# Kernel tuning notes

Hardware: AMD Instinct MI355X
Metric: run time of the kernel (lower is better)

Reference implementation:

```python
import jax, jax.numpy as jnp
import numpy as np

NUM_HEADS = 12
SPARSITY = 0.5

def setup_inputs() -> dict:
    key = jax.random.key(0)
    ks = jax.random.split(key, 5)
    B, N, C = 16, 577, 768
    x = jax.random.normal(ks[0], (B, N, C), dtype=jnp.float32)
    x_original = jax.random.normal(ks[1], (B, N, C), dtype=jnp.float32)
    qkv_w = jax.random.normal(ks[2], (3 * C, C), dtype=jnp.float32) * (C ** -0.5)
    proj_w = jax.random.normal(ks[3], (C, C), dtype=jnp.float32) * (C ** -0.5)
    proj_b = jax.random.normal(ks[4], (C,), dtype=jnp.float32) * 0.01
    return {"x": x, "x_original": x_original, "qkv_w": qkv_w,
            "proj_w": proj_w, "proj_b": proj_b, "num_prop": 57}

def reference(x, x_original, qkv_w, proj_w, proj_b, num_prop):
    B, N, C = x.shape
    H = NUM_HEADS
    hd = C // H
    scale = hd ** -0.5
    # qkv projection (no bias): [B,N,3C] -> q,k,v each [B,H,N,hd]
    qkv = (x @ qkv_w.T).reshape(B, N, 3, H, hd).transpose(2, 0, 3, 1, 4)
    q, k, v = qkv[0], qkv[1], qkv[2]
    attn = jax.nn.softmax(jnp.einsum('bhnd,bhmd->bhnm', q * scale, k), axis=-1)
    # sparsity threshold: keep entries >= the int(N*N*sparsity)-th largest per (b,h)
    if SPARSITY < 1:
        flat = attn.reshape(B, H, N * N)
        desc = -jnp.sort(-flat, axis=-1)  # descending
        sigma = desc[:, :, int(N * N * SPARSITY)][:, :, None, None]
        attn = jnp.where(attn >= sigma, attn, jnp.zeros((), attn.dtype))
    if num_prop > 0:
        K = N - num_prop  # tokens kept (incl. CLS)
        # token importance: max over heads of attention diagonal (excluding CLS)
        diag = jnp.diagonal(attn, axis1=-2, axis2=-1)[:, :, 1:]  # [B,H,N-1]
        token_rank = jnp.argsort(-diag.max(axis=1), axis=1)      # [B,N-1] desc
        index_kept = token_rank[:, :N - 1 - num_prop] + 1        # [B,K-1]
        index_kept = jnp.concatenate(
            [jnp.zeros((B, 1), index_kept.dtype), index_kept], axis=1)  # [B,K]
        # gather kept query rows of attn: [B,H,K,N]
        idx = jnp.broadcast_to(index_kept[:, None, :, None], (B, H, K, N))
        attn_kept = jnp.take_along_axis(attn, idx, axis=2)
        x_original = jnp.take_along_axis(
            x_original, jnp.broadcast_to(index_kept[:, :, None], (B, K, C)), axis=1)
        out = jnp.einsum('bhkn,bhnd->bhkd', attn_kept, v)
        out = out.transpose(0, 2, 1, 3).reshape(B, K, C)
    else:
        out = jnp.einsum('bhnm,bhmd->bhnd', attn, v)
        out = out.transpose(0, 2, 1, 3).reshape(B, N, C)
    out = out @ proj_w.T + proj_b
    return (out, x_original)
```

## Files before the change

kernel.cpp:

```cpp
#include <hip/hip_runtime.h>
#include <cstdint>
#include <cstddef>


namespace {
constexpr int B_  = 16;
constexpr int N_  = 577;
constexpr int C_  = 768;
constexpr int H_  = 12;
constexpr int HD_ = 64;
constexpr int BH_ = B_ * H_;
constexpr int KK_ = N_ - 57;
constexpr unsigned KIDX_ = 166464u;
constexpr int M1_ = B_ * N_;
constexpr int M2_ = B_ * KK_;
}

__device__ __forceinline__ void fma4(const float4& a, const float4& b, float& acc) {
  acc = __builtin_fmaf(a.x, b.x, acc);
  acc = __builtin_fmaf(a.y, b.y, acc);
  acc = __builtin_fmaf(a.z, b.z, acc);
  acc = __builtin_fmaf(a.w, b.w, acc);
}

__global__ __launch_bounds__(256) void qkv_gemm(
    const float* __restrict__ X, const float* __restrict__ W,
    float* __restrict__ qb, float* __restrict__ kb, float* __restrict__ vb) {
  __shared__ __align__(16) float Xs[64][68];
  __shared__ __align__(16) float Ws2[128][68];
  const int m0 = blockIdx.x * 64;
  const int n0 = blockIdx.y * 128;
  const int t = threadIdx.x;
  const int tx = t & 15, ty = t >> 4;
  float acc[4][8] = {};
  for (int k0 = 0; k0 < 768; k0 += 64) {
    __syncthreads();
    {
      const int c = t & 15, r0 = t >> 4;
#pragma unroll
      for (int s = 0; s < 4; s++) {
        int r = r0 + 16 * s;
        int gm = m0 + r;
        float4 v = make_float4(0.f, 0.f, 0.f, 0.f);
        if (gm < M1_) v = *(const float4*)&X[(size_t)gm * 768 + k0 + 4 * c];
        *(float4*)&Xs[r][4 * c] = v;
      }
#pragma unroll
      for (int s = 0; s < 8; s++) {
        int r = r0 + 16 * s;
        float4 v = *(const float4*)&W[(size_t)(n0 + r) * 768 + k0 + 4 * c];
        *(float4*)&Ws2[r][4 * c] = v;
      }
    }
    __syncthreads();
#pragma unroll 2
    for (int d4 = 0; d4 < 16; d4++) {
      float4 a4[4], b4[8];
#pragma unroll
      for (int i = 0; i < 4; i++) a4[i] = *(const float4*)&Xs[tx + 16 * i][4 * d4];
#pragma unroll
      for (int j = 0; j < 8; j++) b4[j] = *(const float4*)&Ws2[ty + 16 * j][4 * d4];
#pragma unroll
      for (int i = 0; i < 4; i++)
#pragma unroll
        for (int j = 0; j < 8; j++) fma4(a4[i], b4[j], acc[i][j]);
    }
  }
  for (int i = 0; i < 4; i++) {
    int gm = m0 + tx + 16 * i;
    if (gm >= M1_) continue;
    int b = gm / N_, n = gm % N_;
    for (int j = 0; j < 8; j++) {
      int gn = n0 + ty + 16 * j;
      int which = gn / C_, rem = gn % C_;
      int h = rem >> 6, d = rem & 63;
      float* dst = (which == 0) ? qb : (which == 1) ? kb : vb;
      dst[(((size_t)(b * H_ + h)) * N_ + n) * HD_ + d] = acc[i][j];
    }
  }
}

__global__ __launch_bounds__(256) void attn_stats(
    const float* __restrict__ qb, const float* __restrict__ kb,
    float* __restrict__ rowmax_g, float* __restrict__ rowsum_g,
    float* __restrict__ ldiag) {
  __shared__ __align__(16) float Qs[64][68];
  __shared__ __align__(16) float Ksf[128][68];
  const int bh = blockIdx.x;
  const int q0 = blockIdx.y * 64;
  const int t = threadIdx.x;
  const int tx = t & 15, ty = t >> 4;
  {
    const int c = t & 15, r0 = t >> 4;
#pragma unroll
    for (int s = 0; s < 4; s++) {
      int r = r0 + 16 * s;
      int gq = q0 + r;
      float4 v = make_float4(0.f, 0.f, 0.f, 0.f);
      if (gq < N_) v = *(const float4*)&qb[((size_t)bh * N_ + gq) * HD_ + 4 * c];
      v.x *= 0.125f; v.y *= 0.125f; v.z *= 0.125f; v.w *= 0.125f;
      *(float4*)&Qs[r][4 * c] = v;
    }
  }
  float m[4], ss[4];
#pragma unroll
  for (int i = 0; i < 4; i++) { m[i] = -INFINITY; ss[i] = 0.f; }
  for (int n0 = 0; n0 < N_; n0 += 128) {
    __syncthreads();
    {
      const int c = t & 15, r0 = t >> 4;
#pragma unroll
      for (int s = 0; s < 8; s++) {
        int r = r0 + 16 * s;
        int gn = n0 + r;
        float4 v = make_float4(0.f, 0.f, 0.f, 0.f);
        if (gn < N_) v = *(const float4*)&kb[((size_t)bh * N_ + gn) * HD_ + 4 * c];
        *(float4*)&Ksf[r][4 * c] = v;
      }
    }
    __syncthreads();
    float l[4][8];
#pragma unroll
    for (int i = 0; i < 4; i++)
#pragma unroll
      for (int j = 0; j < 8; j++) l[i][j] = 0.f;
#pragma unroll 2
    for (int d4 = 0; d4 < 16; d4++) {
      float4 a4[4], b4[8];
#pragma unroll
      for (int i = 0; i < 4; i++) a4[i] = *(const float4*)&Qs[tx + 16 * i][4 * d4];
#pragma unroll
      for (int j = 0; j < 8; j++) b4[j] = *(const float4*)&Ksf[ty + 16 * j][4 * d4];
#pragma unroll
      for (int i = 0; i < 4; i++)
#pragma unroll
        for (int j = 0; j < 8; j++) fma4(a4[i], b4[j], l[i][j]);
    }
#pragma unroll
    for (int i = 0; i < 4; i++) {
      int gq = q0 + tx + 16 * i;
      float tmax = -INFINITY;
#pragma unroll
      for (int j = 0; j < 8; j++)
        if (n0 + ty + 16 * j < N_) tmax = fmaxf(tmax, l[i][j]);
      float mn = fmaxf(m[i], tmax);
      ss[i] *= expf(m[i] - mn);
#pragma unroll
      for (int j = 0; j < 8; j++) {
        int col = n0 + ty + 16 * j;
        if (col < N_) {
          ss[i] += expf(l[i][j] - mn);
          if (col == gq) ldiag[(size_t)bh * N_ + gq] = l[i][j];
        }
      }
      m[i] = mn;
    }
  }
  __syncthreads();
  float* Mred = &Ksf[0][0];
  float* Sred = &Ksf[0][0] + 1024;
#pragma unroll
  for (int i = 0; i < 4; i++) {
    int row = tx + 16 * i;
    Mred[row * 16 + ty] = m[i];
    Sred[row * 16 + ty] = ss[i];
  }
  __syncthreads();
  if (t < 64) {
    int gq = q0 + t;
    if (gq < N_) {
      float M = -INFINITY;
      for (int k = 0; k < 16; k++) M = fmaxf(M, Mred[t * 16 + k]);
      float S = 0.f;
      for (int k = 0; k < 16; k++) S += expf(Mred[t * 16 + k] - M) * Sred[t * 16 + k];
      rowmax_g[(size_t)bh * N_ + gq] = M;
      rowsum_g[(size_t)bh * N_ + gq] = S;
    }
  }
}

template <int MODE>
__global__ __launch_bounds__(256) void hist_pass(
    const float* __restrict__ qb, const float* __restrict__ kb,
    const float* __restrict__ rowmax_g, const float* __restrict__ rowsum_g,
    const unsigned* __restrict__ pfx_in, unsigned* __restrict__ hist_out) {
  constexpr int HB = (MODE == 2) ? 256 : 4096;
  __shared__ __align__(16) float Qs[64][68];
  __shared__ __align__(16) float Ksf[128][68];
  __shared__ unsigned hloc[HB];
  const int bh = blockIdx.x;
  const int q0 = blockIdx.y * 64;
  const int t = threadIdx.x;
  const int tx = t & 15, ty = t >> 4;
  for (int i = t; i < HB; i += 256) hloc[i] = 0u;
  const unsigned pf = (MODE == 0) ? 0u : pfx_in[bh];
  {
    const int c = t & 15, r0 = t >> 4;
#pragma unroll
    for (int s = 0; s < 4; s++) {
      int r = r0 + 16 * s;
      int gq = q0 + r;
      float4 v = make_float4(0.f, 0.f, 0.f, 0.f);
      if (gq < N_) v = *(const float4*)&qb[((size_t)bh * N_ + gq) * HD_ + 4 * c];
      v.x *= 0.125f; v.y *= 0.125f; v.z *= 0.125f; v.w *= 0.125f;
      *(float4*)&Qs[r][4 * c] = v;
    }
  }
  float M[4], inv[4];
#pragma unroll
  for (int i = 0; i < 4; i++) {
    int gq = q0 + tx + 16 * i;
    if (gq < N_) {
      M[i] = rowmax_g[(size_t)bh * N_ + gq];
      inv[i] = 1.f / rowsum_g[(size_t)bh * N_ + gq];
    } else { M[i] = 0.f; inv[i] = 0.f; }
  }
  for (int n0 = 0; n0 < N_; n0 += 128) {
    __syncthreads();
    {
      const int c = t & 15, r0 = t >> 4;
#pragma unroll
      for (int s = 0; s < 8; s++) {
        int r = r0 + 16 * s;
        int gn = n0 + r;
        float4 v = make_float4(0.f, 0.f, 0.f, 0.f);
        if (gn < N_) v = *(const float4*)&kb[((size_t)bh * N_ + gn) * HD_ + 4 * c];
        *(float4*)&Ksf[r][4 * c] = v;
      }
    }
    __syncthreads();
    float l[4][8];
#pragma unroll
    for (int i = 0; i < 4; i++)
#pragma unroll
      for (int j = 0; j < 8; j++) l[i][j] = 0.f;
#pragma unroll 2
    for (int d4 = 0; d4 < 16; d4++) {
      float4 a4[4], b4[8];
#pragma unroll
      for (int i = 0; i < 4; i++) a4[i] = *(const float4*)&Qs[tx + 16 * i][4 * d4];
#pragma unroll
      for (int j = 0; j < 8; j++) b4[j] = *(const float4*)&Ksf[ty + 16 * j][4 * d4];
#pragma unroll
      for (int i = 0; i < 4; i++)
#pragma unroll
        for (int j = 0; j < 8; j++) fma4(a4[i], b4[j], l[i][j]);
    }
#pragma unroll
    for (int i = 0; i < 4; i++) {
      int gq = q0 + tx + 16 * i;
#pragma unroll
      for (int j = 0; j < 8; j++) {
        bool valid = (gq < N_) && (n0 + ty + 16 * j < N_);
        if (MODE == 0) {
          unsigned bin = 0xFFFFu;
          if (valid) {
            float e = expf(l[i][j] - M[i]);
            float v = e * inv[i];
            bin = __float_as_uint(v) >> 20;
          }
          unsigned lead = (unsigned)__builtin_amdgcn_readfirstlane((int)bin);
          unsigned long long mm = __ballot(bin == lead);
          if (bin == lead) {
            if (lead != 0xFFFFu && (t & 63) == (__ffsll((unsigned long long)mm) - 1))
              atomicAdd(&hloc[lead], (unsigned)__popcll(mm));
          } else if (bin != 0xFFFFu) {
            atomicAdd(&hloc[bin], 1u);
          }
        } else if (valid) {
          float e = expf(l[i][j] - M[i]);
          float v = e * inv[i];
          unsigned bits = __float_as_uint(v);
          if (MODE == 1) {
            if ((bits >> 20) == pf) atomicAdd(&hloc[(bits >> 8) & 0xFFFu], 1u);
          } else {
            if ((bits >> 8) == pf) atomicAdd(&hloc[bits & 0xFFu], 1u);
          }
        }
      }
    }
  }
  __syncthreads();
  for (int i = t; i < HB; i += 256)
    if (hloc[i]) atomicAdd(&hist_out[(size_t)bh * HB + i], hloc[i]);
}

__global__ __launch_bounds__(64) void select_level(
    const unsigned* __restrict__ hist, int nbins,
    const unsigned* __restrict__ krem_in, const unsigned* __restrict__ pfx_in,
    unsigned* __restrict__ krem_out, unsigned* __restrict__ pfx_out, int shift) {
  const int bh = blockIdx.x;
  const int l = threadIdx.x;
  const int seg = nbins / 64;
  const unsigned krem = krem_in ? krem_in[bh] : KIDX_;
  const unsigned* hb = hist + (size_t)bh * nbins;
  __shared__ unsigned ps[64];
  unsigned psum = 0;
  int hi = nbins - 1 - l * seg;
  for (int i = 0; i < seg; i++) psum += hb[hi - i];
  ps[l] = psum;
  __syncthreads();
  if (l == 0) {
    unsigned cum = 0, before = 0;
    int bin = 0;
    for (int j = 0; j < 64; j++) {
      if (cum + ps[j] > krem) {
        unsigned c = cum;
        int hj = nbins - 1 - j * seg;
        for (int i = 0; i < seg; i++) {
          unsigned cnt = hb[hj - i];
          if (c + cnt > krem) { bin = hj - i; before = c; break; }
          c += cnt;
        }
        break;
      }
      cum += ps[j];
    }
    unsigned p = pfx_in ? pfx_in[bh] : 0u;
    pfx_out[bh] = (p << shift) | (unsigned)bin;
    krem_out[bh] = krem - before;
  }
}

__global__ __launch_bounds__(576) void rank_kernel(
    const float* __restrict__ ldiag, const float* __restrict__ rowmax_g,
    const float* __restrict__ rowsum_g, const unsigned* __restrict__ sigbits,
    int* __restrict__ kept) {
  const int b = blockIdx.x;
  const int i = threadIdx.x;
  __shared__ float sc[576];
  float s = 0.f;
  for (int h = 0; h < H_; h++) {
    int bh = b * H_ + h;
    float l = ldiag[(size_t)bh * N_ + (i + 1)];
    float M = rowmax_g[(size_t)bh * N_ + (i + 1)];
    float inv = 1.f / rowsum_g[(size_t)bh * N_ + (i + 1)];
    float e = expf(l - M);
    float v = e * inv;
    float sg = __uint_as_float(sigbits[bh]);
    if (v >= sg) s = fmaxf(s, v);
  }
  sc[i] = s;
  __syncthreads();
  int r = 0;
  for (int j = 0; j < 576; j++) {
    float sj = sc[j];
    if (sj > s || (sj == s && j < i)) r++;
  }
  if (r < KK_ - 1) kept[b * KK_ + r + 1] = i + 1;
  if (i == 0) kept[b * KK_] = 0;
}

__global__ __launch_bounds__(256) void gather_x(
    const float* __restrict__ xo, const int* __restrict__ kept,
    float* __restrict__ out2) {
  const int bp = blockIdx.x;
  const int b = bp / KK_, p = bp % KK_;
  const int src = kept[b * KK_ + p];
  const float* s = xo + ((size_t)b * N_ + src) * C_;
  float* d = out2 + (size_t)bp * C_;
  for (int c = threadIdx.x; c < C_; c += 256) d[c] = s[c];
}

__global__ __launch_bounds__(256) void av_kernel(
    const float* __restrict__ qb, const float* __restrict__ kb,
    const float* __restrict__ vb, const int* __restrict__ kept,
    const float* __restrict__ rowmax_g, const float* __restrict__ rowsum_g,
    const unsigned* __restrict__ sigbits, float* __restrict__ out1) {
  __shared__ __align__(16) float Qs[64][68];
  __shared__ __align__(16) float Ksf[64][68];
  __shared__ __align__(16) float Vs[64][68];
  __shared__ int ridx[64];
  __shared__ float Ml[64], Il[64];
  const int bh = blockIdx.x;
  const int p0 = blockIdx.y * 64;
  const int b = bh / H_, h = bh % H_;
  const float sigma = __uint_as_float(sigbits[bh]);
  const int t = threadIdx.x;
  const int tx = t & 15, ty = t >> 4;
  if (t < 64) {
    int pp = p0 + t;
    int r = (pp < KK_) ? kept[b * KK_ + pp] : 0;
    ridx[t] = r;
    Ml[t] = rowmax_g[(size_t)bh * N_ + r];
    Il[t] = 1.f / rowsum_g[(size_t)bh * N_ + r];
  }
  __syncthreads();
  {
    const int c = t & 15, r0 = t >> 4;
#pragma unroll
    for (int s = 0; s < 4; s++) {
      int r = r0 + 16 * s;
      int gq = ridx[r];
      float4 v = *(const float4*)&qb[((size_t)bh * N_ + gq) * HD_ + 4 * c];
      v.x *= 0.125f; v.y *= 0.125f; v.z *= 0.125f; v.w *= 0.125f;
      *(float4*)&Qs[r][4 * c] = v;
    }
  }
  float M[4], inv[4];
#pragma unroll
  for (int i = 0; i < 4; i++) { int row = tx + 16 * i; M[i] = Ml[row]; inv[i] = Il[row]; }
  float acc[4][4] = {};
  for (int n0 = 0; n0 < N_; n0 += 64) {
    __syncthreads();
    {
      const int c = t & 15, r0 = t >> 4;
#pragma unroll
      for (int s = 0; s < 4; s++) {
        int r = r0 + 16 * s;
        int gn = n0 + r;
        float4 kv = make_float4(0.f, 0.f, 0.f, 0.f);
        float4 vv = make_float4(0.f, 0.f, 0.f, 0.f);
        if (gn < N_) {
          kv = *(const float4*)&kb[((size_t)bh * N_ + gn) * HD_ + 4 * c];
          vv = *(const float4*)&vb[((size_t)bh * N_ + gn) * HD_ + 4 * c];
        }
        *(float4*)&Ksf[r][4 * c] = kv;
        *(float4*)&Vs[r][4 * c] = vv;
      }
    }
    __syncthreads();
    float l[4][4];
#pragma unroll
    for (int i = 0; i < 4; i++)
#pragma unroll
      for (int j = 0; j < 4; j++) l[i][j] = 0.f;
#pragma unroll 4
    for (int d4 = 0; d4 < 16; d4++) {
      float4 a4[4], b4[4];
#pragma unroll
      for (int i = 0; i < 4; i++) a4[i] = *(const float4*)&Qs[tx + 16 * i][4 * d4];
#pragma unroll
      for (int j = 0; j < 4; j++) b4[j] = *(const float4*)&Ksf[4 * ty + j][4 * d4];
#pragma unroll
      for (int i = 0; i < 4; i++)
#pragma unroll
        for (int j = 0; j < 4; j++) fma4(a4[i], b4[j], l[i][j]);
    }
    __syncthreads();
#pragma unroll
    for (int i = 0; i < 4; i++) {
      float4 pv4;
      float* pp = (float*)&pv4;
#pragma unroll
      for (int j = 0; j < 4; j++) {
        float e = expf(l[i][j] - M[i]);
        float v = e * inv[i];
        pp[j] = (v >= sigma) ? v : 0.f;
      }
      *(float4*)&Ksf[tx + 16 * i][4 * ty] = pv4;
    }
    __syncthreads();
#pragma unroll 4
    for (int nb = 0; nb < 16; nb++) {
      float4 pa4[4];
#pragma unroll
      for (int i = 0; i < 4; i++) pa4[i] = *(const float4*)&Ksf[tx + 16 * i][4 * nb];
#pragma unroll
      for (int e = 0; e < 4; e++) {
        float4 vv4 = *(const float4*)&Vs[4 * nb + e][4 * ty];
        const float* pa = (const float*)&pa4[0];
#pragma unroll
        for (int i = 0; i < 4; i++) {
          float pvv = ((const float*)&pa4[i])[e];
          acc[i][0] = __builtin_fmaf(pvv, vv4.x, acc[i][0]);
          acc[i][1] = __builtin_fmaf(pvv, vv4.y, acc[i][1]);
          acc[i][2] = __builtin_fmaf(pvv, vv4.z, acc[i][2]);
          acc[i][3] = __builtin_fmaf(pvv, vv4.w, acc[i][3]);
        }
        (void)pa;
      }
    }
  }
#pragma unroll
  for (int i = 0; i < 4; i++) {
    int pp = p0 + tx + 16 * i;
    if (pp >= KK_) continue;
    float4 o = make_float4(acc[i][0], acc[i][1], acc[i][2], acc[i][3]);
    *(float4*)&out1[((size_t)(b * KK_ + pp)) * C_ + h * HD_ + 4 * ty] = o;
  }
}

__global__ __launch_bounds__(256) void proj_gemm(
    const float* __restrict__ Xi, const float* __restrict__ W,
    const float* __restrict__ bias, float* __restrict__ out) {
  __shared__ __align__(16) float Xs[64][68];
  __shared__ __align__(16) float Ws2[128][68];
  const int m0 = blockIdx.x * 64;
  const int n0 = blockIdx.y * 128;
  const int t = threadIdx.x;
  const int tx = t & 15, ty = t >> 4;
  float acc[4][8] = {};
  for (int k0 = 0; k0 < 768; k0 += 64) {
    __syncthreads();
    {
      const int c = t & 15, r0 = t >> 4;
#pragma unroll
      for (int s = 0; s < 4; s++) {
        int r = r0 + 16 * s;
        float4 v = *(const float4*)&Xi[(size_t)(m0 + r) * 768 + k0 + 4 * c];
        *(float4*)&Xs[r][4 * c] = v;
      }
#pragma unroll
      for (int s = 0; s < 8; s++) {
        int r = r0 + 16 * s;
        float4 v = *(const float4*)&W[(size_t)(n0 + r) * 768 + k0 + 4 * c];
        *(float4*)&Ws2[r][4 * c] = v;
      }
    }
    __syncthreads();
#pragma unroll 2
    for (int d4 = 0; d4 < 16; d4++) {
      float4 a4[4], b4[8];
#pragma unroll
      for (int i = 0; i < 4; i++) a4[i] = *(const float4*)&Xs[tx + 16 * i][4 * d4];
#pragma unroll
      for (int j = 0; j < 8; j++) b4[j] = *(const float4*)&Ws2[ty + 16 * j][4 * d4];
#pragma unroll
      for (int i = 0; i < 4; i++)
#pragma unroll
        for (int j = 0; j < 8; j++) fma4(a4[i], b4[j], acc[i][j]);
    }
  }
  for (int i = 0; i < 4; i++) {
    int gm = m0 + tx + 16 * i;
    for (int j = 0; j < 8; j++) {
      int gn = n0 + ty + 16 * j;
      out[(size_t)gm * C_ + gn] = acc[i][j] + bias[gn];
    }
  }
}

extern "C" void kernel_launch(void* const* d_in, const int* in_sizes, int n_in,
                              void* d_out, int out_size, void* d_ws, size_t ws_size,
                              hipStream_t stream) {
  (void)in_sizes; (void)n_in; (void)out_size; (void)ws_size;
  const float* x    = (const float*)d_in[0];
  const float* xo   = (const float*)d_in[1];
  const float* qkvw = (const float*)d_in[2];
  const float* pw   = (const float*)d_in[3];
  const float* pb   = (const float*)d_in[4];

  char* ws = (char*)d_ws;
  size_t off = 0;
  auto alloc = [&](size_t bytes) -> char* {
    char* p = ws + off;
    off += (bytes + 255) & ~(size_t)255;
    return p;
  };
  const size_t szQ    = (size_t)BH_ * N_ * HD_ * 4;
  const size_t szOut1 = (size_t)M2_ * C_ * 4;
  const size_t szRow  = (size_t)BH_ * N_ * 4;
  const size_t szH12  = (size_t)BH_ * 4096 * 4;
  const size_t szH3   = (size_t)BH_ * 256 * 4;

  float* qb     = (float*)alloc(szQ);
  float* kb     = (float*)alloc(szQ);
  float* vb     = (float*)alloc(szQ);
  float* out1   = (float*)alloc(szOut1);
  float* ldiag  = (float*)alloc(szRow);
  float* rowmax = (float*)alloc(szRow);
  float* rowsum = (float*)alloc(szRow);
  unsigned* hist1 = (unsigned*)alloc(szH12);
  unsigned* hist2 = (unsigned*)alloc(szH12);
  unsigned* hist3 = (unsigned*)alloc(szH3);
  unsigned* pfx1  = (unsigned*)alloc(BH_ * 4);
  unsigned* krem1 = (unsigned*)alloc(BH_ * 4);
  unsigned* pfx2  = (unsigned*)alloc(BH_ * 4);
  unsigned* krem2 = (unsigned*)alloc(BH_ * 4);
  unsigned* pfx3  = (unsigned*)alloc(BH_ * 4);
  unsigned* krem3 = (unsigned*)alloc(BH_ * 4);
  int* kept       = (int*)alloc((size_t)B_ * KK_ * 4);

  hipMemsetAsync(hist1, 0, szH12, stream);
  hipMemsetAsync(hist2, 0, szH12, stream);
  hipMemsetAsync(hist3, 0, szH3, stream);

  qkv_gemm<<<dim3(145, 18), 256, 0, stream>>>(x, qkvw, qb, kb, vb);
  attn_stats<<<dim3(BH_, 10), 256, 0, stream>>>(qb, kb, rowmax, rowsum, ldiag);
  hist_pass<0><<<dim3(BH_, 10), 256, 0, stream>>>(qb, kb, rowmax, rowsum, nullptr, hist1);
  select_level<<<BH_, 64, 0, stream>>>(hist1, 4096, nullptr, nullptr, krem1, pfx1, 12);
  hist_pass<1><<<dim3(BH_, 10), 256, 0, stream>>>(qb, kb, rowmax, rowsum, pfx1, hist2);
  select_level<<<BH_, 64, 0, stream>>>(hist2, 4096, krem1, pfx1, krem2, pfx2, 12);
  hist_pass<2><<<dim3(BH_, 10), 256, 0, stream>>>(qb, kb, rowmax, rowsum, pfx2, hist3);
  select_level<<<BH_, 64, 0, stream>>>(hist3, 256, krem2, pfx2, krem3, pfx3, 8);
  rank_kernel<<<B_, 576, 0, stream>>>(ldiag, rowmax, rowsum, pfx3, kept);

  float* outp = (float*)d_out;
  gather_x<<<M2_, 256, 0, stream>>>(xo, kept, outp + (size_t)M2_ * C_);
  av_kernel<<<dim3(BH_, 9), 256, 0, stream>>>(qb, kb, vb, kept, rowmax, rowsum, pfx3, out1);
  proj_gemm<<<dim3(130, 6), 256, 0, stream>>>(out1, pw, pb, outp);
}
```

Measured before the change: 1.801 ms.

## Fuse softmax stats with first histogram, add candidate buffer, enlarge GEMM tiles

The softmax row statistics and the first radix-select histogram now come from one kernel that keeps all logits of a 64-row tile in registers, which removes one full QK^T recompute. The second pass also writes the matching candidate values into a workspace buffer, so the final select level can run from that buffer and the third QK^T pass only runs (gated by a flag) when the buffer overflows. Separately, the QKV and output-projection GEMMs switch to 128x128 tiles with a K step of 32. The trade-offs are higher register pressure (a 5x4x8 logit array and 8x8 accumulators), a large candidate workspace, and more kernels to keep consistent.

```diff
diff --git a/kernel.cpp b/kernel.cpp
--- a/kernel.cpp
+++ b/kernel.cpp
@@ -14,6 +14,8 @@
 constexpr unsigned KIDX_ = 166464u;
 constexpr int M1_ = B_ * N_;
 constexpr int M2_ = B_ * KK_;
+constexpr int CAPMAX_ = 24576;
+constexpr int NT_ = 5;
 }
 
 __device__ __forceinline__ void fma4(const float4& a, const float4& b, float& acc) {
@@ -26,47 +28,43 @@
 __global__ __launch_bounds__(256) void qkv_gemm(
     const float* __restrict__ X, const float* __restrict__ W,
     float* __restrict__ qb, float* __restrict__ kb, float* __restrict__ vb) {
-  __shared__ __align__(16) float Xs[64][68];
-  __shared__ __align__(16) float Ws2[128][68];
-  const int m0 = blockIdx.x * 64;
+  __shared__ __align__(16) float Xs[128][36];
+  __shared__ __align__(16) float Ws2[128][36];
+  const int m0 = blockIdx.x * 128;
   const int n0 = blockIdx.y * 128;
   const int t = threadIdx.x;
   const int tx = t & 15, ty = t >> 4;
-  float acc[4][8] = {};
-  for (int k0 = 0; k0 < 768; k0 += 64) {
+  float acc[8][8] = {};
+  for (int k0 = 0; k0 < 768; k0 += 32) {
     __syncthreads();
     {
-      const int c = t & 15, r0 = t >> 4;
+      const int c = t & 7, r0 = t >> 3;
 #pragma unroll
       for (int s = 0; s < 4; s++) {
-        int r = r0 + 16 * s;
+        int r = r0 + 32 * s;
         int gm = m0 + r;
         float4 v = make_float4(0.f, 0.f, 0.f, 0.f);
         if (gm < M1_) v = *(const float4*)&X[(size_t)gm * 768 + k0 + 4 * c];
         *(float4*)&Xs[r][4 * c] = v;
-      }
-#pragma unroll
-      for (int s = 0; s < 8; s++) {
-        int r = r0 + 16 * s;
-        float4 v = *(const float4*)&W[(size_t)(n0 + r) * 768 + k0 + 4 * c];
-        *(float4*)&Ws2[r][4 * c] = v;
-      }
-    }
-    __syncthreads();
-#pragma unroll 2
-    for (int d4 = 0; d4 < 16; d4++) {
-      float4 a4[4], b4[8];
-#pragma unroll
-      for (int i = 0; i < 4; i++) a4[i] = *(const float4*)&Xs[tx + 16 * i][4 * d4];
+        float4 w = *(const float4*)&W[(size_t)(n0 + r) * 768 + k0 + 4 * c];
+        *(float4*)&Ws2[r][4 * c] = w;
+      }
+    }
+    __syncthreads();
+#pragma unroll
+    for (int d4 = 0; d4 < 8; d4++) {
+      float4 a4[8], b4[8];
+#pragma unroll
+      for (int i = 0; i < 8; i++) a4[i] = *(const float4*)&Xs[tx + 16 * i][4 * d4];
 #pragma unroll
       for (int j = 0; j < 8; j++) b4[j] = *(const float4*)&Ws2[ty + 16 * j][4 * d4];
 #pragma unroll
-      for (int i = 0; i < 4; i++)
+      for (int i = 0; i < 8; i++)
 #pragma unroll
         for (int j = 0; j < 8; j++) fma4(a4[i], b4[j], acc[i][j]);
     }
   }
-  for (int i = 0; i < 4; i++) {
+  for (int i = 0; i < 8; i++) {
     int gm = m0 + tx + 16 * i;
     if (gm >= M1_) continue;
     int b = gm / N_, n = gm % N_;
@@ -80,16 +78,19 @@
   }
 }
 
-__global__ __launch_bounds__(256) void attn_stats(
+__global__ __launch_bounds__(256) void stats_hist1(
     const float* __restrict__ qb, const float* __restrict__ kb,
     float* __restrict__ rowmax_g, float* __restrict__ rowsum_g,
-    float* __restrict__ ldiag) {
+    float* __restrict__ ldiag, unsigned* __restrict__ hist1) {
   __shared__ __align__(16) float Qs[64][68];
   __shared__ __align__(16) float Ksf[128][68];
+  __shared__ unsigned hloc[4096];
+  __shared__ float Mrow[64], Srow[64];
   const int bh = blockIdx.x;
   const int q0 = blockIdx.y * 64;
   const int t = threadIdx.x;
   const int tx = t & 15, ty = t >> 4;
+  for (int i = t; i < 4096; i += 256) hloc[i] = 0u;
   {
     const int c = t & 15, r0 = t >> 4;
 #pragma unroll
@@ -102,10 +103,17 @@
       *(float4*)&Qs[r][4 * c] = v;
     }
   }
-  float m[4], ss[4];
-#pragma unroll
-  for (int i = 0; i < 4; i++) { m[i] = -INFINITY; ss[i] = 0.f; }
-  for (int n0 = 0; n0 < N_; n0 += 128) {
+  float l[NT_][4][8];
+#pragma unroll
+  for (int tt = 0; tt < NT_; tt++)
+#pragma unroll
+    for (int i = 0; i < 4; i++)
+#pragma unroll
+      for (int j = 0; j < 8; j++) l[tt][i][j] = 0.f;
+
+#pragma unroll
+  for (int tt = 0; tt < NT_; tt++) {
+    const int n0 = tt * 128;
     __syncthreads();
     {
       const int c = t & 15, r0 = t >> 4;
@@ -119,11 +127,6 @@
       }
     }
     __syncthreads();
-    float l[4][8];
-#pragma unroll
-    for (int i = 0; i < 4; i++)
-#pragma unroll
-      for (int j = 0; j < 8; j++) l[i][j] = 0.f;
 #pragma unroll 2
     for (int d4 = 0; d4 < 16; d4++) {
       float4 a4[4], b4[8];
@@ -134,155 +137,88 @@
 #pragma unroll
       for (int i = 0; i < 4; i++)
 #pragma unroll
-        for (int j = 0; j < 8; j++) fma4(a4[i], b4[j], l[i][j]);
-    }
+        for (int j = 0; j < 8; j++) fma4(a4[i], b4[j], l[tt][i][j]);
+    }
+  }
+  __syncthreads();
+  float* Mred = &Ksf[0][0];
+  float* Sred = &Ksf[0][0] + 1024;
+#pragma unroll
+  for (int i = 0; i < 4; i++) {
+    float mx = -INFINITY;
+#pragma unroll
+    for (int tt = 0; tt < NT_; tt++)
+#pragma unroll
+      for (int j = 0; j < 8; j++) {
+        int col = tt * 128 + ty + 16 * j;
+        if (col < N_) mx = fmaxf(mx, l[tt][i][j]);
+      }
+    Mred[(tx + 16 * i) * 16 + ty] = mx;
+  }
+  __syncthreads();
+  if (t < 64) {
+    float M = -INFINITY;
+    for (int k = 0; k < 16; k++) M = fmaxf(M, Mred[t * 16 + k]);
+    Mrow[t] = M;
+    if (q0 + t < N_) rowmax_g[(size_t)bh * N_ + q0 + t] = M;
+  }
+  __syncthreads();
+  float Mi_[4];
+#pragma unroll
+  for (int i = 0; i < 4; i++) Mi_[i] = Mrow[tx + 16 * i];
+#pragma unroll
+  for (int i = 0; i < 4; i++) {
+    float s = 0.f;
+#pragma unroll
+    for (int tt = 0; tt < NT_; tt++)
+#pragma unroll
+      for (int j = 0; j < 8; j++) {
+        int col = tt * 128 + ty + 16 * j;
+        if (col < N_) s += expf(l[tt][i][j] - Mi_[i]);
+      }
+    Sred[(tx + 16 * i) * 16 + ty] = s;
+  }
+  __syncthreads();
+  if (t < 64) {
+    float S = 0.f;
+    for (int k = 0; k < 16; k++) S += Sred[t * 16 + k];
+    Srow[t] = S;
+    if (q0 + t < N_) rowsum_g[(size_t)bh * N_ + q0 + t] = S;
+  }
+  __syncthreads();
+  float inv[4];
+#pragma unroll
+  for (int i = 0; i < 4; i++) inv[i] = 1.f / Srow[tx + 16 * i];
+#pragma unroll
+  for (int tt = 0; tt < NT_; tt++) {
 #pragma unroll
     for (int i = 0; i < 4; i++) {
       int gq = q0 + tx + 16 * i;
-      float tmax = -INFINITY;
-#pragma unroll
-      for (int j = 0; j < 8; j++)
-        if (n0 + ty + 16 * j < N_) tmax = fmaxf(tmax, l[i][j]);
-      float mn = fmaxf(m[i], tmax);
-      ss[i] *= expf(m[i] - mn);
 #pragma unroll
       for (int j = 0; j < 8; j++) {
-        int col = n0 + ty + 16 * j;
-        if (col < N_) {
-          ss[i] += expf(l[i][j] - mn);
-          if (col == gq) ldiag[(size_t)bh * N_ + gq] = l[i][j];
-        }
-      }
-      m[i] = mn;
-    }
-  }
-  __syncthreads();
-  float* Mred = &Ksf[0][0];
-  float* Sred = &Ksf[0][0] + 1024;
-#pragma unroll
-  for (int i = 0; i < 4; i++) {
-    int row = tx + 16 * i;
-    Mred[row * 16 + ty] = m[i];
-    Sred[row * 16 + ty] = ss[i];
-  }
-  __syncthreads();
-  if (t < 64) {
-    int gq = q0 + t;
-    if (gq < N_) {
-      float M = -INFINITY;
-      for (int k = 0; k < 16; k++) M = fmaxf(M, Mred[t * 16 + k]);
-      float S = 0.f;
-      for (int k = 0; k < 16; k++) S += expf(Mred[t * 16 + k] - M) * Sred[t * 16 + k];
-      rowmax_g[(size_t)bh * N_ + gq] = M;
-      rowsum_g[(size_t)bh * N_ + gq] = S;
-    }
-  }
-}
-
-template <int MODE>
-__global__ __launch_bounds__(256) void hist_pass(
-    const float* __restrict__ qb, const float* __restrict__ kb,
-    const float* __restrict__ rowmax_g, const float* __restrict__ rowsum_g,
-    const unsigned* __restrict__ pfx_in, unsigned* __restrict__ hist_out) {
-  constexpr int HB = (MODE == 2) ? 256 : 4096;
-  __shared__ __align__(16) float Qs[64][68];
-  __shared__ __align__(16) float Ksf[128][68];
-  __shared__ unsigned hloc[HB];
-  const int bh = blockIdx.x;
-  const int q0 = blockIdx.y * 64;
-  const int t = threadIdx.x;
-  const int tx = t & 15, ty = t >> 4;
-  for (int i = t; i < HB; i += 256) hloc[i] = 0u;
-  const unsigned pf = (MODE == 0) ? 0u : pfx_in[bh];
-  {
-    const int c = t & 15, r0 = t >> 4;
-#pragma unroll
-    for (int s = 0; s < 4; s++) {
-      int r = r0 + 16 * s;
-      int gq = q0 + r;
-      float4 v = make_float4(0.f, 0.f, 0.f, 0.f);
-      if (gq < N_) v = *(const float4*)&qb[((size_t)bh * N_ + gq) * HD_ + 4 * c];
-      v.x *= 0.125f; v.y *= 0.125f; v.z *= 0.125f; v.w *= 0.125f;
-      *(float4*)&Qs[r][4 * c] = v;
-    }
-  }
-  float M[4], inv[4];
-#pragma unroll
-  for (int i = 0; i < 4; i++) {
-    int gq = q0 + tx + 16 * i;
-    if (gq < N_) {
-      M[i] = rowmax_g[(size_t)bh * N_ + gq];
-      inv[i] = 1.f / rowsum_g[(size_t)bh * N_ + gq];
-    } else { M[i] = 0.f; inv[i] = 0.f; }
-  }
-  for (int n0 = 0; n0 < N_; n0 += 128) {
-    __syncthreads();
-    {
-      const int c = t & 15, r0 = t >> 4;
-#pragma unroll
-      for (int s = 0; s < 8; s++) {
-        int r = r0 + 16 * s;
-        int gn = n0 + r;
-        float4 v = make_float4(0.f, 0.f, 0.f, 0.f);
-        if (gn < N_) v = *(const float4*)&kb[((size_t)bh * N_ + gn) * HD_ + 4 * c];
-        *(float4*)&Ksf[r][4 * c] = v;
-      }
-    }
-    __syncthreads();
-    float l[4][8];
-#pragma unroll
-    for (int i = 0; i < 4; i++)
-#pragma unroll
-      for (int j = 0; j < 8; j++) l[i][j] = 0.f;
-#pragma unroll 2
-    for (int d4 = 0; d4 < 16; d4++) {
-      float4 a4[4], b4[8];
-#pragma unroll
-      for (int i = 0; i < 4; i++) a4[i] = *(const float4*)&Qs[tx + 16 * i][4 * d4];
-#pragma unroll
-      for (int j = 0; j < 8; j++) b4[j] = *(const float4*)&Ksf[ty + 16 * j][4 * d4];
-#pragma unroll
-      for (int i = 0; i < 4; i++)
-#pragma unroll
-        for (int j = 0; j < 8; j++) fma4(a4[i], b4[j], l[i][j]);
-    }
-#pragma unroll
-    for (int i = 0; i < 4; i++) {
-      int gq = q0 + tx + 16 * i;
-#pragma unroll
-      for (int j = 0; j < 8; j++) {
-        bool valid = (gq < N_) && (n0 + ty + 16 * j < N_);
-        if (MODE == 0) {
-          unsigned bin = 0xFFFFu;
-          if (valid) {
-            float e = expf(l[i][j] - M[i]);
-            float v = e * inv[i];
-            bin = __float_as_uint(v) >> 20;
-          }
-          unsigned lead = (unsigned)__builtin_amdgcn_readfirstlane((int)bin);
-          unsigned long long mm = __ballot(bin == lead);
-          if (bin == lead) {
-            if (lead != 0xFFFFu && (t & 63) == (__ffsll((unsigned long long)mm) - 1))
-              atomicAdd(&hloc[lead], (unsigned)__popcll(mm));
-          } else if (bin != 0xFFFFu) {
-            atomicAdd(&hloc[bin], 1u);
-          }
-        } else if (valid) {
-          float e = expf(l[i][j] - M[i]);
+        int col = tt * 128 + ty + 16 * j;
+        bool valid = (gq < N_) && (col < N_);
+        unsigned bin = 0xFFFFu;
+        if (valid) {
+          float e = expf(l[tt][i][j] - Mi_[i]);
           float v = e * inv[i];
-          unsigned bits = __float_as_uint(v);
-          if (MODE == 1) {
-            if ((bits >> 20) == pf) atomicAdd(&hloc[(bits >> 8) & 0xFFFu], 1u);
-          } else {
-            if ((bits >> 8) == pf) atomicAdd(&hloc[bits & 0xFFu], 1u);
-          }
-        }
-      }
-    }
-  }
-  __syncthreads();
-  for (int i = t; i < HB; i += 256)
-    if (hloc[i]) atomicAdd(&hist_out[(size_t)bh * HB + i], hloc[i]);
+          bin = __float_as_uint(v) >> 20;
+          if (col == gq) ldiag[(size_t)bh * N_ + gq] = l[tt][i][j];
+        }
+        unsigned lead = (unsigned)__builtin_amdgcn_readfirstlane((int)bin);
+        unsigned long long mm = __ballot(bin == lead);
+        if (bin == lead) {
+          if (lead != 0xFFFFu && (t & 63) == (__ffsll((unsigned long long)mm) - 1))
+            atomicAdd(&hloc[lead], (unsigned)__popcll(mm));
+        } else if (bin != 0xFFFFu) {
+          atomicAdd(&hloc[bin], 1u);
+        }
+      }
+    }
+  }
+  __syncthreads();
+  for (int i = t; i < 4096; i += 256)
+    if (hloc[i]) atomicAdd(&hist1[(size_t)bh * 4096 + i], hloc[i]);
 }
 
 __global__ __launch_bounds__(64) void select_level(
@@ -319,6 +255,328 @@
     unsigned p = pfx_in ? pfx_in[bh] : 0u;
     pfx_out[bh] = (p << shift) | (unsigned)bin;
     krem_out[bh] = krem - before;
+  }
+}
+
+__global__ __launch_bounds__(256) void cand_pass(
+    const float* __restrict__ qb, const float* __restrict__ kb,
+    const float* __restrict__ rowmax_g, const float* __restrict__ rowsum_g,
+    const unsigned* __restrict__ pfx1, unsigned* __restrict__ candCnt,
+    unsigned* __restrict__ cand, int cap, unsigned* __restrict__ hist2) {
+  __shared__ __align__(16) float Qs[64][68];
+  __shared__ __align__(16) float Ksf[128][68];
+  __shared__ unsigned hloc[4096];
+  const int bh = blockIdx.x;
+  const int q0 = blockIdx.y * 64;
+  const int t = threadIdx.x;
+  const int tx = t & 15, ty = t >> 4;
+  for (int i = t; i < 4096; i += 256) hloc[i] = 0u;
+  const unsigned pf = pfx1[bh];
+  {
+    const int c = t & 15, r0 = t >> 4;
+#pragma unroll
+    for (int s = 0; s < 4; s++) {
+      int r = r0 + 16 * s;
+      int gq = q0 + r;
+      float4 v = make_float4(0.f, 0.f, 0.f, 0.f);
+      if (gq < N_) v = *(const float4*)&qb[((size_t)bh * N_ + gq) * HD_ + 4 * c];
+      v.x *= 0.125f; v.y *= 0.125f; v.z *= 0.125f; v.w *= 0.125f;
+      *(float4*)&Qs[r][4 * c] = v;
+    }
+  }
+  float M[4], inv[4];
+#pragma unroll
+  for (int i = 0; i < 4; i++) {
+    int gq = q0 + tx + 16 * i;
+    if (gq < N_) {
+      M[i] = rowmax_g[(size_t)bh * N_ + gq];
+      inv[i] = 1.f / rowsum_g[(size_t)bh * N_ + gq];
+    } else { M[i] = 0.f; inv[i] = 0.f; }
+  }
+  for (int n0 = 0; n0 < N_; n0 += 128) {
+    __syncthreads();
+    {
+      const int c = t & 15, r0 = t >> 4;
+#pragma unroll
+      for (int s = 0; s < 8; s++) {
+        int r = r0 + 16 * s;
+        int gn = n0 + r;
+        float4 v = make_float4(0.f, 0.f, 0.f, 0.f);
+        if (gn < N_) v = *(const float4*)&kb[((size_t)bh * N_ + gn) * HD_ + 4 * c];
+        *(float4*)&Ksf[r][4 * c] = v;
+      }
+    }
+    __syncthreads();
+    float l[4][8];
+#pragma unroll
+    for (int i = 0; i < 4; i++)
+#pragma unroll
+      for (int j = 0; j < 8; j++) l[i][j] = 0.f;
+#pragma unroll 2
+    for (int d4 = 0; d4 < 16; d4++) {
+      float4 a4[4], b4[8];
+#pragma unroll
+      for (int i = 0; i < 4; i++) a4[i] = *(const float4*)&Qs[tx + 16 * i][4 * d4];
+#pragma unroll
+      for (int j = 0; j < 8; j++) b4[j] = *(const float4*)&Ksf[ty + 16 * j][4 * d4];
+#pragma unroll
+      for (int i = 0; i < 4; i++)
+#pragma unroll
+        for (int j = 0; j < 8; j++) fma4(a4[i], b4[j], l[i][j]);
+    }
+#pragma unroll
+    for (int i = 0; i < 4; i++) {
+      int gq = q0 + tx + 16 * i;
+#pragma unroll
+      for (int j = 0; j < 8; j++) {
+        bool valid = (gq < N_) && (n0 + ty + 16 * j < N_);
+        unsigned bits = 0u;
+        bool match = false;
+        if (valid) {
+          float e = expf(l[i][j] - M[i]);
+          float v = e * inv[i];
+          bits = __float_as_uint(v);
+          match = ((bits >> 20) == pf);
+        }
+        unsigned long long mm = __ballot(match);
+        if (mm) {
+          int leader = __ffsll((unsigned long long)mm) - 1;
+          unsigned base = 0;
+          if ((t & 63) == leader)
+            base = atomicAdd(&candCnt[bh], (unsigned)__popcll(mm));
+          base = (unsigned)__shfl((int)base, leader, 64);
+          if (match) {
+            unsigned rank = (unsigned)__popcll(mm & ((1ull << (t & 63)) - 1ull));
+            unsigned idx = base + rank;
+            if ((int)idx < cap) cand[(size_t)bh * CAPMAX_ + idx] = bits;
+            atomicAdd(&hloc[(bits >> 8) & 0xFFFu], 1u);
+          }
+        }
+      }
+    }
+  }
+  __syncthreads();
+  for (int i = t; i < 4096; i += 256)
+    if (hloc[i]) atomicAdd(&hist2[(size_t)bh * 4096 + i], hloc[i]);
+}
+
+__global__ __launch_bounds__(256) void select_mid(
+    const unsigned* __restrict__ cand, const unsigned* __restrict__ candCnt,
+    int cap, const unsigned* __restrict__ krem1, const unsigned* __restrict__ pfx1,
+    const unsigned* __restrict__ hist2, unsigned* __restrict__ krem2,
+    unsigned* __restrict__ pfx2, unsigned* __restrict__ sigbits,
+    unsigned* __restrict__ flag) {
+  const int bh = blockIdx.x;
+  const int t = threadIdx.x;
+  __shared__ unsigned h[4096];
+  __shared__ unsigned ps[256];
+  __shared__ unsigned sh_bin, sh_krem;
+  const unsigned cnt = candCnt[bh];
+  const unsigned krem = krem1[bh];
+  const unsigned p1 = pfx1[bh];
+  if (cap > 0 && cnt <= (unsigned)cap) {
+    const unsigned* cb = cand + (size_t)bh * CAPMAX_;
+    for (int i = t; i < 1024; i += 256) h[i] = 0u;
+    __syncthreads();
+    for (unsigned i = t; i < cnt; i += 256) atomicAdd(&h[(cb[i] >> 10) & 1023u], 1u);
+    __syncthreads();
+    { unsigned s = 0; int hi = 1023 - t * 4;
+      for (int k = 0; k < 4; k++) s += h[hi - k];
+      ps[t] = s; }
+    __syncthreads();
+    if (t == 0) {
+      unsigned cum = 0, before = 0; int bin = 0;
+      for (int j = 0; j < 256; j++) {
+        unsigned pj = ps[j];
+        if (cum + pj > krem) {
+          unsigned c = cum; int hj = 1023 - j * 4;
+          for (int k = 0; k < 4; k++) {
+            unsigned cc = h[hj - k];
+            if (c + cc > krem) { bin = hj - k; before = c; break; }
+            c += cc;
+          }
+          break;
+        }
+        cum += pj;
+      }
+      sh_bin = (unsigned)bin; sh_krem = krem - before;
+    }
+    __syncthreads();
+    const unsigned binA = sh_bin;
+    const unsigned kremA = sh_krem;
+    __syncthreads();
+    for (int i = t; i < 1024; i += 256) h[i] = 0u;
+    __syncthreads();
+    for (unsigned i = t; i < cnt; i += 256) {
+      unsigned c = cb[i];
+      if (((c >> 10) & 1023u) == binA) atomicAdd(&h[c & 1023u], 1u);
+    }
+    __syncthreads();
+    { unsigned s = 0; int hi = 1023 - t * 4;
+      for (int k = 0; k < 4; k++) s += h[hi - k];
+      ps[t] = s; }
+    __syncthreads();
+    if (t == 0) {
+      unsigned cum = 0; int bin = 0;
+      for (int j = 0; j < 256; j++) {
+        unsigned pj = ps[j];
+        if (cum + pj > kremA) {
+          unsigned c = cum; int hj = 1023 - j * 4;
+          for (int k = 0; k < 4; k++) {
+            unsigned cc = h[hj - k];
+            if (c + cc > kremA) { bin = hj - k; break; }
+            c += cc;
+          }
+          break;
+        }
+        cum += pj;
+      }
+      sigbits[bh] = (p1 << 20) | (binA << 10) | (unsigned)bin;
+      flag[bh] = 0u;
+    }
+  } else {
+    const unsigned* hb = hist2 + (size_t)bh * 4096;
+    { unsigned s = 0; int hi = 4095 - t * 16;
+      for (int k = 0; k < 16; k++) s += hb[hi - k];
+      ps[t] = s; }
+    __syncthreads();
+    if (t == 0) {
+      unsigned cum = 0, before = 0; int bin = 0;
+      for (int j = 0; j < 256; j++) {
+        unsigned pj = ps[j];
+        if (cum + pj > krem) {
+          unsigned c = cum; int hj = 4095 - j * 16;
+          for (int k = 0; k < 16; k++) {
+            unsigned cc = hb[hj - k];
+            if (c + cc > krem) { bin = hj - k; before = c; break; }
+            c += cc;
+          }
+          break;
+        }
+        cum += pj;
+      }
+      pfx2[bh] = (p1 << 12) | (unsigned)bin;
+      krem2[bh] = krem - before;
+      flag[bh] = 1u;
+    }
+  }
+}
+
+__global__ __launch_bounds__(256) void hist_l3(
+    const float* __restrict__ qb, const float* __restrict__ kb,
+    const float* __restrict__ rowmax_g, const float* __restrict__ rowsum_g,
+    const unsigned* __restrict__ pfx2, const unsigned* __restrict__ flag,
+    unsigned* __restrict__ hist3) {
+  const int bh = blockIdx.x;
+  if (flag[bh] == 0u) return;
+  __shared__ __align__(16) float Qs[64][68];
+  __shared__ __align__(16) float Ksf[128][68];
+  __shared__ unsigned hloc[256];
+  const int q0 = blockIdx.y * 64;
+  const int t = threadIdx.x;
+  const int tx = t & 15, ty = t >> 4;
+  if (t < 256) hloc[t] = 0u;
+  const unsigned pf = pfx2[bh];
+  {
+    const int c = t & 15, r0 = t >> 4;
+#pragma unroll
+    for (int s = 0; s < 4; s++) {
+      int r = r0 + 16 * s;
+      int gq = q0 + r;
+      float4 v = make_float4(0.f, 0.f, 0.f, 0.f);
+      if (gq < N_) v = *(const float4*)&qb[((size_t)bh * N_ + gq) * HD_ + 4 * c];
+      v.x *= 0.125f; v.y *= 0.125f; v.z *= 0.125f; v.w *= 0.125f;
+      *(float4*)&Qs[r][4 * c] = v;
+    }
+  }
+  float M[4], inv[4];
+#pragma unroll
+  for (int i = 0; i < 4; i++) {
+    int gq = q0 + tx + 16 * i;
+    if (gq < N_) {
+      M[i] = rowmax_g[(size_t)bh * N_ + gq];
+      inv[i] = 1.f / rowsum_g[(size_t)bh * N_ + gq];
+    } else { M[i] = 0.f; inv[i] = 0.f; }
+  }
+  for (int n0 = 0; n0 < N_; n0 += 128) {
+    __syncthreads();
+    {
+      const int c = t & 15, r0 = t >> 4;
+#pragma unroll
+      for (int s = 0; s < 8; s++) {
+        int r = r0 + 16 * s;
+        int gn = n0 + r;
+        float4 v = make_float4(0.f, 0.f, 0.f, 0.f);
+        if (gn < N_) v = *(const float4*)&kb[((size_t)bh * N_ + gn) * HD_ + 4 * c];
+        *(float4*)&Ksf[r][4 * c] = v;
+      }
+    }
+    __syncthreads();
+    float l[4][8];
+#pragma unroll
+    for (int i = 0; i < 4; i++)
+#pragma unroll
+      for (int j = 0; j < 8; j++) l[i][j] = 0.f;
+#pragma unroll 2
+    for (int d4 = 0; d4 < 16; d4++) {
+      float4 a4[4], b4[8];
+#pragma unroll
+      for (int i = 0; i < 4; i++) a4[i] = *(const float4*)&Qs[tx + 16 * i][4 * d4];
+#pragma unroll
+      for (int j = 0; j < 8; j++) b4[j] = *(const float4*)&Ksf[ty + 16 * j][4 * d4];
+#pragma unroll
+      for (int i = 0; i < 4; i++)
+#pragma unroll
+        for (int j = 0; j < 8; j++) fma4(a4[i], b4[j], l[i][j]);
+    }
+#pragma unroll
+    for (int i = 0; i < 4; i++) {
+      int gq = q0 + tx + 16 * i;
+#pragma unroll
+      for (int j = 0; j < 8; j++) {
+        if ((gq < N_) && (n0 + ty + 16 * j < N_)) {
+          float e = expf(l[i][j] - M[i]);
+          float v = e * inv[i];
+          unsigned bits = __float_as_uint(v);
+          if ((bits >> 8) == pf) atomicAdd(&hloc[bits & 0xFFu], 1u);
+        }
+      }
+    }
+  }
+  __syncthreads();
+  if (t < 256 && hloc[t]) atomicAdd(&hist3[(size_t)bh * 256 + t], hloc[t]);
+}
+
+__global__ __launch_bounds__(64) void select_l3(
+    const unsigned* __restrict__ hist3, const unsigned* __restrict__ krem2,
+    const unsigned* __restrict__ pfx2, const unsigned* __restrict__ flag,
+    unsigned* __restrict__ sigbits) {
+  const int bh = blockIdx.x;
+  if (flag[bh] == 0u) return;
+  const int l = threadIdx.x;
+  const unsigned krem = krem2[bh];
+  const unsigned* hb = hist3 + (size_t)bh * 256;
+  __shared__ unsigned ps[64];
+  unsigned psum = 0;
+  int hi = 255 - l * 4;
+  for (int i = 0; i < 4; i++) psum += hb[hi - i];
+  ps[l] = psum;
+  __syncthreads();
+  if (l == 0) {
+    unsigned cum = 0; int bin = 0;
+    for (int j = 0; j < 64; j++) {
+      if (cum + ps[j] > krem) {
+        unsigned c = cum; int hj = 255 - j * 4;
+        for (int i = 0; i < 4; i++) {
+          unsigned cnt = hb[hj - i];
+          if (c + cnt > krem) { bin = hj - i; break; }
+          c += cnt;
+        }
+        break;
+      }
+      cum += ps[j];
+    }
+    sigbits[bh] = (pfx2[bh] << 8) | (unsigned)bin;
   }
 }
 
@@ -459,7 +717,6 @@
 #pragma unroll
       for (int e = 0; e < 4; e++) {
         float4 vv4 = *(const float4*)&Vs[4 * nb + e][4 * ty];
-        const float* pa = (const float*)&pa4[0];
 #pragma unroll
         for (int i = 0; i < 4; i++) {
           float pvv = ((const float*)&pa4[i])[e];
@@ -468,7 +725,6 @@
           acc[i][2] = __builtin_fmaf(pvv, vv4.z, acc[i][2]);
           acc[i][3] = __builtin_fmaf(pvv, vv4.w, acc[i][3]);
         }
-        (void)pa;
       }
     }
   }
@@ -484,45 +740,41 @@
 __global__ __launch_bounds__(256) void proj_gemm(
     const float* __restrict__ Xi, const float* __restrict__ W,
     const float* __restrict__ bias, float* __restrict__ out) {
-  __shared__ __align__(16) float Xs[64][68];
-  __shared__ __align__(16) float Ws2[128][68];
-  const int m0 = blockIdx.x * 64;
+  __shared__ __align__(16) float Xs[128][36];
+  __shared__ __align__(16) float Ws2[128][36];
+  const int m0 = blockIdx.x * 128;
   const int n0 = blockIdx.y * 128;
   const int t = threadIdx.x;
   const int tx = t & 15, ty = t >> 4;
-  float acc[4][8] = {};
-  for (int k0 = 0; k0 < 768; k0 += 64) {
+  float acc[8][8] = {};
+  for (int k0 = 0; k0 < 768; k0 += 32) {
     __syncthreads();
     {
-      const int c = t & 15, r0 = t >> 4;
+      const int c = t & 7, r0 = t >> 3;
 #pragma unroll
       for (int s = 0; s < 4; s++) {
-        int r = r0 + 16 * s;
+        int r = r0 + 32 * s;
         float4 v = *(const float4*)&Xi[(size_t)(m0 + r) * 768 + k0 + 4 * c];
         *(float4*)&Xs[r][4 * c] = v;
-      }
-#pragma unroll
-      for (int s = 0; s < 8; s++) {
-        int r = r0 + 16 * s;
-        float4 v = *(const float4*)&W[(size_t)(n0 + r) * 768 + k0 + 4 * c];
-        *(float4*)&Ws2[r][4 * c] = v;
-      }
-    }
-    __syncthreads();
-#pragma unroll 2
-    for (int d4 = 0; d4 < 16; d4++) {
-      float4 a4[4], b4[8];
-#pragma unroll
-      for (int i = 0; i < 4; i++) a4[i] = *(const float4*)&Xs[tx + 16 * i][4 * d4];
+        float4 w = *(const float4*)&W[(size_t)(n0 + r) * 768 + k0 + 4 * c];
+        *(float4*)&Ws2[r][4 * c] = w;
+      }
+    }
+    __syncthreads();
+#pragma unroll
+    for (int d4 = 0; d4 < 8; d4++) {
+      float4 a4[8], b4[8];
+#pragma unroll
+      for (int i = 0; i < 8; i++) a4[i] = *(const float4*)&Xs[tx + 16 * i][4 * d4];
 #pragma unroll
       for (int j = 0; j < 8; j++) b4[j] = *(const float4*)&Ws2[ty + 16 * j][4 * d4];
 #pragma unroll
-      for (int i = 0; i < 4; i++)
+      for (int i = 0; i < 8; i++)
 #pragma unroll
         for (int j = 0; j < 8; j++) fma4(a4[i], b4[j], acc[i][j]);
     }
   }
-  for (int i = 0; i < 4; i++) {
+  for (int i = 0; i < 8; i++) {
     int gm = m0 + tx + 16 * i;
     for (int j = 0; j < 8; j++) {
       int gn = n0 + ty + 16 * j;
@@ -534,7 +786,7 @@
 extern "C" void kernel_launch(void* const* d_in, const int* in_sizes, int n_in,
                               void* d_out, int out_size, void* d_ws, size_t ws_size,
                               hipStream_t stream) {
-  (void)in_sizes; (void)n_in; (void)out_size; (void)ws_size;
+  (void)in_sizes; (void)n_in; (void)out_size;
   const float* x    = (const float*)d_in[0];
   const float* xo   = (const float*)d_in[1];
   const float* qkvw = (const float*)d_in[2];
@@ -568,26 +820,33 @@
   unsigned* krem1 = (unsigned*)alloc(BH_ * 4);
   unsigned* pfx2  = (unsigned*)alloc(BH_ * 4);
   unsigned* krem2 = (unsigned*)alloc(BH_ * 4);
-  unsigned* pfx3  = (unsigned*)alloc(BH_ * 4);
-  unsigned* krem3 = (unsigned*)alloc(BH_ * 4);
+  unsigned* sigb  = (unsigned*)alloc(BH_ * 4);
+  unsigned* flag  = (unsigned*)alloc(BH_ * 4);
+  unsigned* candCnt = (unsigned*)alloc(BH_ * 4);
   int* kept       = (int*)alloc((size_t)B_ * KK_ * 4);
+  size_t off_nocand = off;
+  unsigned* cand  = (unsigned*)alloc((size_t)BH_ * CAPMAX_ * 4);
+  const int cap = (ws_size >= off) ? CAPMAX_ : 0;
+  if (cap == 0) cand = (unsigned*)(ws + off_nocand - 256);
 
   hipMemsetAsync(hist1, 0, szH12, stream);
   hipMemsetAsync(hist2, 0, szH12, stream);
   hipMemsetAsync(hist3, 0, szH3, stream);
-
-  qkv_gemm<<<dim3(145, 18), 256, 0, stream>>>(x, qkvw, qb, kb, vb);
-  attn_stats<<<dim3(BH_, 10), 256, 0, stream>>>(qb, kb, rowmax, rowsum, ldiag);
-  hist_pass<0><<<dim3(BH_, 10), 256, 0, stream>>>(qb, kb, rowmax, rowsum, nullptr, hist1);
+  hipMemsetAsync(candCnt, 0, BH_ * 4, stream);
+
+  qkv_gemm<<<dim3(73, 18), 256, 0, stream>>>(x, qkvw, qb, kb, vb);
+  stats_hist1<<<dim3(BH_, 10), 256, 0, stream>>>(qb, kb, rowmax, rowsum, ldiag, hist1);
   select_level<<<BH_, 64, 0, stream>>>(hist1, 4096, nullptr, nullptr, krem1, pfx1, 12);
-  hist_pass<1><<<dim3(BH_, 10), 256, 0, stream>>>(qb, kb, rowmax, rowsum, pfx1, hist2);
-  select_level<<<BH_, 64, 0, stream>>>(hist2, 4096, krem1, pfx1, krem2, pfx2, 12);
-  hist_pass<2><<<dim3(BH_, 10), 256, 0, stream>>>(qb, kb, rowmax, rowsum, pfx2, hist3);
-  select_level<<<BH_, 64, 0, stream>>>(hist3, 256, krem2, pfx2, krem3, pfx3, 8);
-  rank_kernel<<<B_, 576, 0, stream>>>(ldiag, rowmax, rowsum, pfx3, kept);
+  cand_pass<<<dim3(BH_, 10), 256, 0, stream>>>(qb, kb, rowmax, rowsum, pfx1,
+                                               candCnt, cand, cap, hist2);
+  select_mid<<<BH_, 256, 0, stream>>>(cand, candCnt, cap, krem1, pfx1, hist2,
+                                      krem2, pfx2, sigb, flag);
+  hist_l3<<<dim3(BH_, 10), 256, 0, stream>>>(qb, kb, rowmax, rowsum, pfx2, flag, hist3);
+  select_l3<<<BH_, 64, 0, stream>>>(hist3, krem2, pfx2, flag, sigb);
+  rank_kernel<<<B_, 576, 0, stream>>>(ldiag, rowmax, rowsum, sigb, kept);
 
   float* outp = (float*)d_out;
   gather_x<<<M2_, 256, 0, stream>>>(xo, kept, outp + (size_t)M2_ * C_);
-  av_kernel<<<dim3(BH_, 9), 256, 0, stream>>>(qb, kb, vb, kept, rowmax, rowsum, pfx3, out1);
-  proj_gemm<<<dim3(130, 6), 256, 0, stream>>>(out1, pw, pb, outp);
-}
+  av_kernel<<<dim3(BH_, 9), 256, 0, stream>>>(qb, kb, vb, kept, rowmax, rowsum, sigb, out1);
+  proj_gemm<<<dim3(65, 6), 256, 0, stream>>>(out1, pw, pb, outp);
+}
```

After: 3.609 ms. +100.4%, slower.
